# Kernel tuning notes

Hardware: AMD Instinct MI355X
Metric: run time of the kernel (lower is better)

## Reference

```python
import jax, jax.numpy as jnp
import numpy as np

MAX_TOP_K = 3
NUM_EXPERTS = 64
B, S, D = 4, 4096, 4096
H = D // 2


def setup_inputs() -> dict:
    key = jax.random.key(0)
    k0, k1, k2, k3 = jax.random.split(key, 4)
    x = jax.random.normal(k0, (B, S, D), dtype=jnp.float32)
    W = jax.random.normal(k1, (D, NUM_EXPERTS), dtype=jnp.float32) * 0.1
    # top_k_predictor: Linear(D, D//2) -> ReLU -> Linear(D//2, 1) -> Sigmoid
    W1 = jax.random.normal(k2, (D, H), dtype=jnp.float32) * (1.0 / np.sqrt(D))
    b1 = jnp.zeros((H,), dtype=jnp.float32)
    W2 = jax.random.normal(k3, (H, 1), dtype=jnp.float32) * (1.0 / np.sqrt(H))
    b2 = jnp.zeros((1,), dtype=jnp.float32)
    return {"x": x, "W": W, "W1": W1, "b1": b1, "W2": W2, "b2": b2}


def reference(x, W, W1, b1, W2, b2):
    b, s, d = x.shape
    x_flat = x.reshape(-1, d)                                  # [N, D]
    n = x_flat.shape[0]

    # small predictor MLP -> per-token dynamic k
    h = jax.nn.relu(x_flat @ W1 + b1)                          # [N, H]
    top_k_scores = jax.nn.sigmoid(h @ W2 + b2)[:, 0]           # [N]
    dynamic_top_k = jnp.clip(
        jnp.round(top_k_scores * MAX_TOP_K) + 1.0, 1.0, float(MAX_TOP_K)
    ).astype(jnp.int32)                                        # [N]

    # gating matmul + softmax + top-k
    gate_probs = jax.nn.softmax(x_flat @ W, axis=-1)           # [N, E]
    top_k_probs, top_k_indices = jax.lax.top_k(gate_probs, MAX_TOP_K)  # [N, K]

    # per-token dynamic-k mask and renormalize
    k_mask = jnp.arange(MAX_TOP_K)[None, :] < dynamic_top_k[:, None]   # [N, K]
    top_k_probs = top_k_probs * k_mask.astype(top_k_probs.dtype)
    top_k_weights = top_k_probs / (top_k_probs.sum(-1, keepdims=True) + 1e-8)

    # routing mask: 1 where expert is in top-k AND its (masked) weight > 0
    rows = jnp.arange(n)[:, None]                              # [N, 1]
    routing_mask = jnp.zeros((n, NUM_EXPERTS), top_k_weights.dtype).at[
        rows, top_k_indices
    ].set((top_k_weights > 0).astype(top_k_weights.dtype))     # [N, E]

    return (
        top_k_weights,
        top_k_indices,
        routing_mask.reshape(b, s, NUM_EXPERTS),
        dynamic_top_k,
    )
```

## Files before the change

### kernel.cpp

```cpp
#include <hip/hip_runtime.h>
#include <hip/hip_bf16.h>
#include <math.h>

#define DD   4096
#define HH   2048
#define NE   64
#define BK   32
#define NT   16
#define GM   32
#define GMP  (GM + 2)
#define NEP  (NE + 2)

typedef __attribute__((ext_vector_type(8))) short bf16x8;
typedef __attribute__((ext_vector_type(4))) float f32x4;

__device__ __forceinline__ void async16(void* lds, const void* g) {
    __builtin_amdgcn_global_load_lds(
        (const __attribute__((address_space(1))) unsigned int*)g,
        (__attribute__((address_space(3))) unsigned int*)lds, 16, 0, 0);
}

__device__ __forceinline__ void split2(float a, float b, unsigned& hi, unsigned& lo) {
    __hip_bfloat162 h = __float22bfloat162_rn(make_float2(a, b));
    float2 hf = __bfloat1622float2(h);
    __hip_bfloat162 l = __float22bfloat162_rn(make_float2(a - hf.x, b - hf.y));
    __builtin_memcpy(&hi, &h, 4);
    __builtin_memcpy(&lo, &l, 4);
}

__global__ __launch_bounds__(256) void split_xf(
    const float* __restrict__ x, uint4* __restrict__ xfh, uint4* __restrict__ xfl)
{
    const int t = threadIdx.x;
    const int mt = blockIdx.x >> 7;
    const int ks = blockIdx.x & 127;
#pragma unroll
    for (int s2 = 0; s2 < 2; ++s2) {
        int s = t + s2 * 256;
        int fb = s >> 6, ln = s & 63;
        int row = mt * 128 + fb * 16 + (ln & 15);
        int k   = ks * 32 + (ln >> 4) * 8;
        const float* g = x + (size_t)row * DD + k;
        float4 a = *(const float4*)g, b = *(const float4*)(g + 4);
        unsigned h0, l0, h1, l1, h2, l2, h3, l3;
        split2(a.x, a.y, h0, l0); split2(a.z, a.w, h1, l1);
        split2(b.x, b.y, h2, l2); split2(b.z, b.w, h3, l3);
        size_t idx = ((size_t)blockIdx.x * 8 + fb) * 64 + ln;
        xfh[idx] = make_uint4(h0, h1, h2, h3);
        xfl[idx] = make_uint4(l0, l1, l2, l3);
    }
}

__global__ __launch_bounds__(256) void split_w1t(
    const float* __restrict__ W1,
    unsigned short* __restrict__ th, unsigned short* __restrict__ tl)
{
    __shared__ float ts[32][33];
    const int n0 = blockIdx.x * 32, k0 = blockIdx.y * 32;
    const int t = threadIdx.x;
    {
        int r = t >> 3, c4 = (t & 7) * 4;
        float4 v = *(const float4*)&W1[(size_t)(k0 + r) * HH + n0 + c4];
        ts[r][c4] = v.x; ts[r][c4 + 1] = v.y; ts[r][c4 + 2] = v.z; ts[r][c4 + 3] = v.w;
    }
    __syncthreads();
    int n = t >> 3, kk = (t & 7) * 4;
    float f0 = ts[kk][n], f1 = ts[kk + 1][n], f2 = ts[kk + 2][n], f3 = ts[kk + 3][n];
    unsigned h0, l0, h1, l1;
    split2(f0, f1, h0, l0); split2(f2, f3, h1, l1);
    *(uint2*)&th[(size_t)(n0 + n) * DD + k0 + kk] = make_uint2(h0, h1);
    *(uint2*)&tl[(size_t)(n0 + n) * DD + k0 + kk] = make_uint2(l0, l1);
}

template<bool PRE_A>
__global__ __launch_bounds__(256, 3) void pred_mfma(
    const float* __restrict__ x,
    const unsigned short* __restrict__ xh, const unsigned short* __restrict__ xl,
    const unsigned short* __restrict__ w1th, const unsigned short* __restrict__ w1tl,
    const float* __restrict__ b1, const float* __restrict__ W2,
    double* __restrict__ pl)
{
    __shared__ __align__(16) char lds[32768];

    const int t = threadIdx.x, wv = t >> 6, ln = t & 63;
    const int lin = blockIdx.x;
    const int sub = lin >> 3;
    const int ntile = (lin & 7) * 2 + (sub & 1);
    const int mtile = sub >> 1;
    const int m0 = mtile * 128, n0 = ntile * 128;
    const int frow = ln & 15;
    const int fkb  = (ln >> 4) * 8;

    f32x4 acc[4][4];
#pragma unroll
    for (int i = 0; i < 4; ++i)
#pragma unroll
        for (int j = 0; j < 4; ++j) acc[i][j] = (f32x4){0.f, 0.f, 0.f, 0.f};

    const int mb = (wv & 1) * 4, nb = (wv >> 1) * 4;

    if (PRE_A) {
        char* Bh = lds;
        char* Bl = lds + 8192;

        const unsigned short* bsrc = (wv & 2) ? w1tl : w1th;
        const int fb0 = (wv & 1) * 4;
        char* bdst = ((wv & 2) ? Bl : Bh) + fb0 * 1024;
        const unsigned short* bg =
            bsrc + (size_t)(n0 + fb0 * 16 + frow) * DD + fkb;

        const uint4* gh = (const uint4*)xh + ((size_t)mtile * 1024 + mb) * 64 + ln;
        const uint4* gl = (const uint4*)xl + ((size_t)mtile * 1024 + mb) * 64 + ln;

        bf16x8 ah[4], al[4];

#pragma unroll
        for (int q = 0; q < 4; ++q)
            async16(bdst + q * 1024, bg + (size_t)q * 16 * DD);
#pragma unroll
        for (int i = 0; i < 4; ++i) {
            ah[i] = *(const bf16x8*)(gh + i * 64);
            al[i] = *(const bf16x8*)(gl + i * 64);
        }

        for (int ks = 0; ks < 128; ++ks) {
            __syncthreads();

            bf16x8 bfh[4], bfl[4];
#pragma unroll
            for (int j = 0; j < 4; ++j) {
                bfh[j] = *(const bf16x8*)(Bh + (nb + j) * 1024 + ln * 16);
                bfl[j] = *(const bf16x8*)(Bl + (nb + j) * 1024 + ln * 16);
            }
            __syncthreads();

            const bool more = (ks + 1 < 128);
            if (more) {
#pragma unroll
                for (int q = 0; q < 4; ++q)
                    async16(bdst + q * 1024,
                            bg + (size_t)q * 16 * DD + (ks + 1) * BK);
            }

#pragma unroll
            for (int i = 0; i < 4; ++i)
#pragma unroll
                for (int j = 0; j < 4; ++j) {
                    acc[i][j] = __builtin_amdgcn_mfma_f32_16x16x32_bf16(ah[i], bfh[j], acc[i][j], 0, 0, 0);
                    acc[i][j] = __builtin_amdgcn_mfma_f32_16x16x32_bf16(ah[i], bfl[j], acc[i][j], 0, 0, 0);
                }
            if (more) {
#pragma unroll
                for (int i = 0; i < 4; ++i)
                    ah[i] = *(const bf16x8*)(gh + (size_t)(ks + 1) * 512 + i * 64);
            }
#pragma unroll
            for (int i = 0; i < 4; ++i)
#pragma unroll
                for (int j = 0; j < 4; ++j)
                    acc[i][j] = __builtin_amdgcn_mfma_f32_16x16x32_bf16(al[i], bfh[j], acc[i][j], 0, 0, 0);
            if (more) {
#pragma unroll
                for (int i = 0; i < 4; ++i)
                    al[i] = *(const bf16x8*)(gl + (size_t)(ks + 1) * 512 + i * 64);
            }
        }
    } else {
        char* Ah = lds;
        char* Al = lds + 8192;
        char* Bh = lds + 16384;
        char* Bl = lds + 24576;
        const unsigned short* gBh = w1th + (size_t)(n0 + frow) * DD + fkb;
        const unsigned short* gBl = w1tl + (size_t)(n0 + frow) * DD + fkb;

        for (int kc = 0; kc < DD; kc += BK) {
#pragma unroll
            for (int q = 0; q < 2; ++q) {
                int fb = wv * 2 + q;
                async16(Bh + fb * 1024, gBh + (size_t)fb * 16 * DD + kc);
                async16(Bl + fb * 1024, gBl + (size_t)fb * 16 * DD + kc);
            }
#pragma unroll
            for (int s2 = 0; s2 < 2; ++s2) {
                int s = t + s2 * 256;
                int fb = s >> 6, sl = s & 63;
                int row = fb * 16 + (sl & 15), kb = (sl >> 4) * 8;
                const float* g = x + (size_t)(m0 + row) * DD + kc + kb;
                float4 a = *(const float4*)g, b = *(const float4*)(g + 4);
                unsigned h0, l0, h1, l1, h2, l2, h3, l3;
                split2(a.x, a.y, h0, l0); split2(a.z, a.w, h1, l1);
                split2(b.x, b.y, h2, l2); split2(b.z, b.w, h3, l3);
                *(uint4*)(Ah + s * 16) = make_uint4(h0, h1, h2, h3);
                *(uint4*)(Al + s * 16) = make_uint4(l0, l1, l2, l3);
            }
            __syncthreads();

            bf16x8 afh[4], afl[4], bfh[4], bfl[4];
#pragma unroll
            for (int i = 0; i < 4; ++i) {
                afh[i] = *(const bf16x8*)(Ah + (mb + i) * 1024 + ln * 16);
                afl[i] = *(const bf16x8*)(Al + (mb + i) * 1024 + ln * 16);
                bfh[i] = *(const bf16x8*)(Bh + (nb + i) * 1024 + ln * 16);
                bfl[i] = *(const bf16x8*)(Bl + (nb + i) * 1024 + ln * 16);
            }
#pragma unroll
            for (int i = 0; i < 4; ++i)
#pragma unroll
                for (int j = 0; j < 4; ++j) {
                    acc[i][j] = __builtin_amdgcn_mfma_f32_16x16x32_bf16(afh[i], bfh[j], acc[i][j], 0, 0, 0);
                    acc[i][j] = __builtin_amdgcn_mfma_f32_16x16x32_bf16(afh[i], bfl[j], acc[i][j], 0, 0, 0);
                    acc[i][j] = __builtin_amdgcn_mfma_f32_16x16x32_bf16(afl[i], bfh[j], acc[i][j], 0, 0, 0);
                }
            __syncthreads();
        }
    }

    __syncthreads();
    double* redd = (double*)lds;
    const int mh = wv & 1, nh = wv >> 1;
    float b1v[4], w2v[4];
#pragma unroll
    for (int j = 0; j < 4; ++j) {
        int col = n0 + nh * 64 + j * 16 + frow;
        b1v[j] = b1[col];
        w2v[j] = W2[col];
    }
#pragma unroll
    for (int i = 0; i < 4; ++i)
#pragma unroll
        for (int r = 0; r < 4; ++r) {
            double s = 0.0;
#pragma unroll
            for (int j = 0; j < 4; ++j) {
                float h = acc[i][j][r] + b1v[j];
                h = fmaxf(h, 0.f);
                s += (double)h * (double)w2v[j];
            }
#pragma unroll
            for (int o = 1; o < 16; o <<= 1) s += __shfl_xor(s, o, 64);
            if (frow == 0)
                redd[nh * 128 + mh * 64 + i * 16 + (ln >> 4) * 4 + r] = s;
        }
    __syncthreads();
    if (t < 128)
        pl[(size_t)(m0 + t) * NT + ntile] = redd[t] + redd[128 + t];
}

__global__ __launch_bounds__(256) void pred_gemm(
    const float* __restrict__ x, const float* __restrict__ W1,
    const float* __restrict__ b1, const float* __restrict__ W2,
    double* __restrict__ pl)
{
    __shared__ float As[BK][128];
    __shared__ float Bs[BK][128];
    __shared__ double red[128][NT + 1];

    const int ht = blockIdx.x;
    const int tm = blockIdx.y;
    const int t  = threadIdx.x;
    const int tx = t & 15, ty = t >> 4;
    const int h0 = ht * 128;
    const int m0 = tm * 128;

    float acc[8][8];
#pragma unroll
    for (int i = 0; i < 8; ++i)
#pragma unroll
        for (int j = 0; j < 8; ++j) acc[i][j] = 0.f;

    const int arow = t >> 1, acol = (t & 1) << 4;
    const int brow = t >> 3, bcol = (t & 7) << 4;
    const float* xrow = x  + (size_t)(m0 + arow) * DD + acol;
    const float* wrow = W1 + (size_t)brow * HH + h0 + bcol;

    for (int k0 = 0; k0 < DD; k0 += BK) {
        float4 a4[4], b4[4];
        const float4* ap = (const float4*)(xrow + k0);
#pragma unroll
        for (int i = 0; i < 4; ++i) a4[i] = ap[i];
        const float4* bp = (const float4*)(wrow + (size_t)k0 * HH);
#pragma unroll
        for (int i = 0; i < 4; ++i) b4[i] = bp[i];
        __syncthreads();
#pragma unroll
        for (int i = 0; i < 4; ++i) {
            As[acol + i * 4 + 0][arow] = a4[i].x;
            As[acol + i * 4 + 1][arow] = a4[i].y;
            As[acol + i * 4 + 2][arow] = a4[i].z;
            As[acol + i * 4 + 3][arow] = a4[i].w;
        }
#pragma unroll
        for (int i = 0; i < 4; ++i)
            *(float4*)&Bs[brow][bcol + i * 4] = b4[i];
        __syncthreads();
#pragma unroll 8
        for (int kk = 0; kk < BK; ++kk) {
            float4 a0  = *(const float4*)&As[kk][ty * 8];
            float4 a1  = *(const float4*)&As[kk][ty * 8 + 4];
            float4 bb0 = *(const float4*)&Bs[kk][tx * 8];
            float4 bb1 = *(const float4*)&Bs[kk][tx * 8 + 4];
            float av[8] = {a0.x, a0.y, a0.z, a0.w, a1.x, a1.y, a1.z, a1.w};
            float bv[8] = {bb0.x, bb0.y, bb0.z, bb0.w, bb1.x, bb1.y, bb1.z, bb1.w};
#pragma unroll
            for (int i = 0; i < 8; ++i)
#pragma unroll
                for (int j = 0; j < 8; ++j)
                    acc[i][j] = fmaf(av[i], bv[j], acc[i][j]);
        }
    }
    __syncthreads();
#pragma unroll
    for (int r = 0; r < 8; ++r) {
        double s = 0.0;
#pragma unroll
        for (int c = 0; c < 8; ++c) {
            int h = h0 + tx * 8 + c;
            float v = acc[r][c] + b1[h];
            v = v > 0.f ? v : 0.f;
            s += (double)v * (double)W2[h];
        }
        red[ty * 8 + r][tx] = s;
    }
    __syncthreads();
    if (t < 128) {
        double s = 0.0;
#pragma unroll
        for (int j = 0; j < NT; ++j) s += red[t][j];
        pl[(size_t)(m0 + t) * NT + ht] = s;
    }
}

__global__ __launch_bounds__(256) void gate_fused(
    const float* __restrict__ x, const float* __restrict__ W,
    const double* __restrict__ pl, const float* __restrict__ b2,
    float* __restrict__ out, int Ntok)
{
    __shared__ __align__(16) char smem[(BK * GMP + BK * NEP) * 8];
    double (*Asd)[GMP] = (double(*)[GMP])smem;
    double (*Bsd)[NEP] = (double(*)[NEP])(smem + BK * GMP * 8);
    double (*Dm)[NE + 1] = (double(*)[NE + 1])smem;

    const int tm = blockIdx.x;
    const int t  = threadIdx.x;
    const int tx = t & 15, ty = t >> 4;
    const int m0 = tm * GM;

    double acc[2][4];
#pragma unroll
    for (int i = 0; i < 2; ++i)
#pragma unroll
        for (int j = 0; j < 4; ++j) acc[i][j] = 0.0;

    const int arow = t >> 3, acol = (t & 7) * 4;
    const int brow = t >> 3, bcol = (t & 7) * 8;
    const float* xrow = x + (size_t)(m0 + arow) * DD + acol;
    const float* wrow = W + (size_t)brow * NE + bcol;

    float4 a4  = *(const float4*)xrow;
    float4 b40 = *(const float4*)wrow;
    float4 b41 = *(const float4*)(wrow + 4);

    for (int k0 = 0; k0 < DD; k0 += BK) {
        __syncthreads();
        Asd[acol + 0][arow] = (double)a4.x;
        Asd[acol + 1][arow] = (double)a4.y;
        Asd[acol + 2][arow] = (double)a4.z;
        Asd[acol + 3][arow] = (double)a4.w;
        Bsd[brow][bcol + 0] = (double)b40.x;
        Bsd[brow][bcol + 1] = (double)b40.y;
        Bsd[brow][bcol + 2] = (double)b40.z;
        Bsd[brow][bcol + 3] = (double)b40.w;
        Bsd[brow][bcol + 4] = (double)b41.x;
        Bsd[brow][bcol + 5] = (double)b41.y;
        Bsd[brow][bcol + 6] = (double)b41.z;
        Bsd[brow][bcol + 7] = (double)b41.w;
        __syncthreads();

        if (k0 + BK < DD) {
            a4  = *(const float4*)(xrow + k0 + BK);
            b40 = *(const float4*)(wrow + (size_t)(k0 + BK) * NE);
            b41 = *(const float4*)(wrow + (size_t)(k0 + BK) * NE + 4);
        }

#pragma unroll 8
        for (int kk = 0; kk < BK; ++kk) {
            double2 av  = *(const double2*)&Asd[kk][ty * 2];
            double2 bv0 = *(const double2*)&Bsd[kk][tx * 4];
            double2 bv1 = *(const double2*)&Bsd[kk][tx * 4 + 2];
            double bv[4] = {bv0.x, bv0.y, bv1.x, bv1.y};
#pragma unroll
            for (int j = 0; j < 4; ++j) {
                acc[0][j] = fma(av.x, bv[j], acc[0][j]);
                acc[1][j] = fma(av.y, bv[j], acc[1][j]);
            }
        }
    }

    __syncthreads();
#pragma unroll
    for (int r = 0; r < 2; ++r)
#pragma unroll
        for (int c = 0; c < 4; ++c)
            Dm[ty * 2 + r][tx * 4 + c] = acc[r][c];
    __syncthreads();

    const int wave = t >> 6;
    const int lane = t & 63;
    const double b2v = (double)b2[0];

    for (int i = 0; i < 8; ++i) {
        const int tl = wave * 8 + i;
        const int token = m0 + tl;
        double g = Dm[tl][lane];

        double mx = g;
#pragma unroll
        for (int o = 32; o > 0; o >>= 1) mx = fmax(mx, __shfl_xor(mx, o, 64));
        double e = exp(g - mx);
        double s = e;
#pragma unroll
        for (int o = 32; o > 0; o >>= 1) s += __shfl_xor(s, o, 64);
        double p = e / s;

        double pv = p; int pi = lane;
        double vt[3]; int it[3];
#pragma unroll
        for (int j = 0; j < 3; ++j) {
            double v = pv; int idx = pi;
#pragma unroll
            for (int o = 32; o > 0; o >>= 1) {
                double ov = __shfl_xor(v, o, 64);
                int    oi = __shfl_xor(idx, o, 64);
                if (ov > v || (ov == v && oi < idx)) { v = ov; idx = oi; }
            }
            vt[j] = v; it[j] = idx;
            if (lane == idx) pv = -1.0;
        }

        double plv = (lane < NT) ? pl[(size_t)token * NT + lane] : 0.0;
#pragma unroll
        for (int o = 32; o > 0; o >>= 1) plv += __shfl_xor(plv, o, 64);
        double logit = plv + b2v;
        double score = 1.0 / (1.0 + exp(-logit));
        int k = (int)rint(score * 3.0) + 1;
        k = k < 1 ? 1 : (k > 3 ? 3 : k);

        double wmask[3]; double wsum = 0.0;
#pragma unroll
        for (int j = 0; j < 3; ++j) { wmask[j] = (j < k) ? vt[j] : 0.0; wsum += wmask[j]; }
        double denom = wsum + 1e-8;
        float wn[3];
#pragma unroll
        for (int j = 0; j < 3; ++j) wn[j] = (float)(wmask[j] / denom);

        float mval = 0.f;
#pragma unroll
        for (int j = 0; j < 3; ++j)
            if (it[j] == lane && wn[j] > 0.f) mval = 1.f;

        out[(size_t)6 * Ntok + (size_t)token * NE + lane] = mval;
        if (lane < 3) {
            out[(size_t)token * 3 + lane] = wn[lane];
            out[(size_t)3 * Ntok + (size_t)token * 3 + lane] = (float)it[lane];
        }
        if (lane == 0) out[(size_t)70 * Ntok + token] = (float)k;
    }
}

extern "C" void kernel_launch(void* const* d_in, const int* in_sizes, int n_in,
                              void* d_out, int out_size, void* d_ws, size_t ws_size,
                              hipStream_t stream)
{
    const float* x  = (const float*)d_in[0];
    const float* W  = (const float*)d_in[1];
    const float* W1 = (const float*)d_in[2];
    const float* b1 = (const float*)d_in[3];
    const float* W2 = (const float*)d_in[4];
    const float* b2 = (const float*)d_in[5];
    float* out = (float*)d_out;

    const int Ntok = in_sizes[0] / DD;

    double* pl = (double*)d_ws;
    const size_t pl_b   = (size_t)Ntok * NT * sizeof(double);
    const size_t o_w1h  = (pl_b + 255) & ~(size_t)255;
    const size_t w1_b   = (size_t)DD * HH * 2;
    const size_t o_w1l  = o_w1h + w1_b;
    const size_t o_xh   = o_w1l + w1_b;
    const size_t x_b    = (size_t)Ntok * DD * 2;
    const size_t o_xl   = o_xh + x_b;
    const size_t need_w1   = o_xh;
    const size_t need_full = o_xl + x_b;

    const bool ok128 = (Ntok % 128) == 0;

    if (ok128 && ws_size >= need_w1) {
        unsigned short* w1th = (unsigned short*)((char*)d_ws + o_w1h);
        unsigned short* w1tl = (unsigned short*)((char*)d_ws + o_w1l);
        split_w1t<<<dim3(HH / 32, DD / 32), 256, 0, stream>>>(W1, w1th, w1tl);
        if (ws_size >= need_full) {
            unsigned short* xfh = (unsigned short*)((char*)d_ws + o_xh);
            unsigned short* xfl = (unsigned short*)((char*)d_ws + o_xl);
            split_xf<<<Ntok, 256, 0, stream>>>(x, (uint4*)xfh, (uint4*)xfl);
            pred_mfma<true><<<16 * (Ntok / 128), 256, 0, stream>>>(
                x, xfh, xfl, w1th, w1tl, b1, W2, pl);
        } else {
            pred_mfma<false><<<16 * (Ntok / 128), 256, 0, stream>>>(
                x, nullptr, nullptr, w1th, w1tl, b1, W2, pl);
        }
    } else {
        pred_gemm<<<dim3(NT, Ntok / 128), 256, 0, stream>>>(x, W1, b1, W2, pl);
    }

    gate_fused<<<Ntok / GM, 256, 0, stream>>>(x, W, pl, b2, out, Ntok);
}
```

Baseline: 1.703 ms.

## Double-buffer W1 LDS tiles in predictor GEMM and store gate tiles as float

The predictor GEMM's W1 tile staging becomes a two-slot LDS ping-pong. The next tile's async global-to-LDS loads are issued before the current tile is read, and one explicit vmcnt wait plus barrier per iteration replaces the two __syncthreads. The gate GEMM now keeps its x and W tiles in LDS as float instead of double and converts to double on read. This halves LDS footprint and store traffic but adds conversions in the inner loop. The hand-written vmcnt counts depend on the exact number of loads in flight, so a miscount could cause a race.

```diff
diff --git a/kernel.cpp b/kernel.cpp
--- a/kernel.cpp
+++ b/kernel.cpp
@@ -8,8 +8,6 @@
 #define BK   32
 #define NT   16
 #define GM   32
-#define GMP  (GM + 2)
-#define NEP  (NE + 2)
 
 typedef __attribute__((ext_vector_type(8))) short bf16x8;
 typedef __attribute__((ext_vector_type(4))) float f32x4;
@@ -100,14 +98,10 @@
     const int mb = (wv & 1) * 4, nb = (wv >> 1) * 4;
 
     if (PRE_A) {
-        char* Bh = lds;
-        char* Bl = lds + 8192;
-
         const unsigned short* bsrc = (wv & 2) ? w1tl : w1th;
-        const int fb0 = (wv & 1) * 4;
-        char* bdst = ((wv & 2) ? Bl : Bh) + fb0 * 1024;
+        const int roleoff = ((wv & 2) ? 8192 : 0) + (wv & 1) * 4096;
         const unsigned short* bg =
-            bsrc + (size_t)(n0 + fb0 * 16 + frow) * DD + fkb;
+            bsrc + (size_t)(n0 + (wv & 1) * 64 + frow) * DD + fkb;
 
         const uint4* gh = (const uint4*)xh + ((size_t)mtile * 1024 + mb) * 64 + ln;
         const uint4* gl = (const uint4*)xl + ((size_t)mtile * 1024 + mb) * 64 + ln;
@@ -116,30 +110,34 @@
 
 #pragma unroll
         for (int q = 0; q < 4; ++q)
-            async16(bdst + q * 1024, bg + (size_t)q * 16 * DD);
+            async16(lds + roleoff + q * 1024, bg + (size_t)q * 16 * DD);
+        __builtin_amdgcn_sched_barrier(0);
 #pragma unroll
         for (int i = 0; i < 4; ++i) {
             ah[i] = *(const bf16x8*)(gh + i * 64);
             al[i] = *(const bf16x8*)(gl + i * 64);
         }
+        asm volatile("s_waitcnt vmcnt(8)" ::: "memory");
+        __builtin_amdgcn_s_barrier();
 
         for (int ks = 0; ks < 128; ++ks) {
-            __syncthreads();
+            const int rb = (ks & 1) << 14;
+            const int sb = rb ^ 16384;
+            const bool more = (ks + 1 < 128);
+
+            if (more) {
+#pragma unroll
+                for (int q = 0; q < 4; ++q)
+                    async16(lds + sb + roleoff + q * 1024,
+                            bg + (size_t)q * 16 * DD + (ks + 1) * BK);
+            }
+            __builtin_amdgcn_sched_barrier(0);
 
             bf16x8 bfh[4], bfl[4];
 #pragma unroll
             for (int j = 0; j < 4; ++j) {
-                bfh[j] = *(const bf16x8*)(Bh + (nb + j) * 1024 + ln * 16);
-                bfl[j] = *(const bf16x8*)(Bl + (nb + j) * 1024 + ln * 16);
-            }
-            __syncthreads();
-
-            const bool more = (ks + 1 < 128);
-            if (more) {
-#pragma unroll
-                for (int q = 0; q < 4; ++q)
-                    async16(bdst + q * 1024,
-                            bg + (size_t)q * 16 * DD + (ks + 1) * BK);
+                bfh[j] = *(const bf16x8*)(lds + rb + (nb + j) * 1024 + ln * 16);
+                bfl[j] = *(const bf16x8*)(lds + rb + 8192 + (nb + j) * 1024 + ln * 16);
             }
 
 #pragma unroll
@@ -163,6 +161,8 @@
 #pragma unroll
                 for (int i = 0; i < 4; ++i)
                     al[i] = *(const bf16x8*)(gl + (size_t)(ks + 1) * 512 + i * 64);
+                asm volatile("s_waitcnt vmcnt(8)" ::: "memory");
+                __builtin_amdgcn_s_barrier();
             }
         }
     } else {
@@ -335,9 +335,9 @@
     const double* __restrict__ pl, const float* __restrict__ b2,
     float* __restrict__ out, int Ntok)
 {
-    __shared__ __align__(16) char smem[(BK * GMP + BK * NEP) * 8];
-    double (*Asd)[GMP] = (double(*)[GMP])smem;
-    double (*Bsd)[NEP] = (double(*)[NEP])(smem + BK * GMP * 8);
+    __shared__ __align__(16) char smem[GM * (NE + 1) * sizeof(double)];
+    float (*As)[GM] = (float(*)[GM])smem;
+    float (*Bs)[NE] = (float(*)[NE])(smem + BK * GM * 4);
     double (*Dm)[NE + 1] = (double(*)[NE + 1])smem;
 
     const int tm = blockIdx.x;
@@ -362,18 +362,12 @@
 
     for (int k0 = 0; k0 < DD; k0 += BK) {
         __syncthreads();
-        Asd[acol + 0][arow] = (double)a4.x;
-        Asd[acol + 1][arow] = (double)a4.y;
-        Asd[acol + 2][arow] = (double)a4.z;
-        Asd[acol + 3][arow] = (double)a4.w;
-        Bsd[brow][bcol + 0] = (double)b40.x;
-        Bsd[brow][bcol + 1] = (double)b40.y;
-        Bsd[brow][bcol + 2] = (double)b40.z;
-        Bsd[brow][bcol + 3] = (double)b40.w;
-        Bsd[brow][bcol + 4] = (double)b41.x;
-        Bsd[brow][bcol + 5] = (double)b41.y;
-        Bsd[brow][bcol + 6] = (double)b41.z;
-        Bsd[brow][bcol + 7] = (double)b41.w;
+        As[acol + 0][arow] = a4.x;
+        As[acol + 1][arow] = a4.y;
+        As[acol + 2][arow] = a4.z;
+        As[acol + 3][arow] = a4.w;
+        *(float4*)&Bs[brow][bcol]     = b40;
+        *(float4*)&Bs[brow][bcol + 4] = b41;
         __syncthreads();
 
         if (k0 + BK < DD) {
@@ -384,14 +378,14 @@
 
 #pragma unroll 8
         for (int kk = 0; kk < BK; ++kk) {
-            double2 av  = *(const double2*)&Asd[kk][ty * 2];
-            double2 bv0 = *(const double2*)&Bsd[kk][tx * 4];
-            double2 bv1 = *(const double2*)&Bsd[kk][tx * 4 + 2];
-            double bv[4] = {bv0.x, bv0.y, bv1.x, bv1.y};
+            double a0 = (double)As[kk][ty * 2];
+            double a1 = (double)As[kk][ty * 2 + 1];
+            float4 b = *(const float4*)&Bs[kk][tx * 4];
+            double bv[4] = {(double)b.x, (double)b.y, (double)b.z, (double)b.w};
 #pragma unroll
             for (int j = 0; j < 4; ++j) {
-                acc[0][j] = fma(av.x, bv[j], acc[0][j]);
-                acc[1][j] = fma(av.y, bv[j], acc[1][j]);
+                acc[0][j] = fma(a0, bv[j], acc[0][j]);
+                acc[1][j] = fma(a1, bv[j], acc[1][j]);
             }
         }
     }
```

New measurement: 1.549 ms. -9.0%, faster.
